# Kernel optimization log

Hardware: AMD Instinct MI355X
Metric: run time of the kernel (lower is better)

The kernel has to match this reference:

```python
import jax, jax.numpy as jnp
import numpy as np

DT = 1.0          # integration timestep (ms)
SIGMA = 0.5       # gauss_std for surrogate (unused in pure fwd spike)
AMPLITUDE = 0.3   # dampening_factor
N = 50000         # neurons
R = 4             # receptor types
D = 5             # max_delay
E = 5000000       # recurrent synapses
B = 4             # batch


def setup_inputs() -> dict:
    key = jax.random.key(0)
    ks = jax.random.split(key, 20)
    f = jnp.float32
    inputs = jax.random.normal(ks[0], (B, N * R), f) * 0.1
    # z_buf holds binary spikes for the last D steps
    z_buf = jax.random.bernoulli(ks[1], 0.05, (B, N * D)).astype(f)
    v = jax.random.uniform(ks[2], (B, N), f, 0.0, 1.0)
    r = jnp.zeros((B, N), f)
    asc_1 = jax.random.normal(ks[3], (B, N), f)
    asc_2 = jax.random.normal(ks[4], (B, N), f)
    psc_rise = jax.random.normal(ks[5], (B, N * R), f) * 0.5
    psc = jax.random.normal(ks[6], (B, N * R), f)
    rec_w = jax.random.normal(ks[7], (E,), f) * 0.01
    rec_rows = jax.random.randint(ks[8], (E,), 0, N * R, jnp.int32)
    rec_cols = jax.random.randint(ks[9], (E,), 0, N * D, jnp.int32)
    syn_decay = jax.random.uniform(ks[10], (N, R), f, 0.5, 0.99)
    psc_initial = jax.random.uniform(ks[11], (N, R), f, 0.1, 1.0)
    t_ref = jax.random.uniform(ks[12], (N,), f, 1.0, 4.0)
    asc_amps = jax.random.normal(ks[13], (N, 2), f)
    k = jax.random.normal(ks[14], (N, 2), f)  # inv-sigmoid space, read via sigmoid
    v_th = jnp.ones((N,), f)
    e_l = jnp.zeros((N,), f)
    v_reset = jnp.zeros((N,), f)
    g = jax.random.uniform(ks[15], (N,), f, 0.1, 1.0)
    decay = jax.random.uniform(ks[16], (N,), f, 0.8, 0.99)
    current_factor = jax.random.uniform(ks[17], (N,), f, 0.1, 1.0)
    voltage_scale = jnp.ones((N,), f) * 20.0
    voltage_offset = jnp.ones((N,), f) * -70.0
    return dict(inputs=inputs, z_buf=z_buf, v=v, r=r, asc_1=asc_1, asc_2=asc_2,
                psc_rise=psc_rise, psc=psc, rec_w=rec_w, rec_rows=rec_rows,
                rec_cols=rec_cols, syn_decay=syn_decay, psc_initial=psc_initial,
                t_ref=t_ref, asc_amps=asc_amps, k=k, v_th=v_th, e_l=e_l,
                v_reset=v_reset, g=g, decay=decay, current_factor=current_factor,
                voltage_scale=voltage_scale, voltage_offset=voltage_offset)


def _step(inputs, z_buf, v, r, asc_1, asc_2, psc_rise, psc,
          rec_w, rec_rows, rec_cols, syn_decay, psc_initial, t_ref,
          asc_amps, k, v_th, e_l, v_reset, g, decay, current_factor,
          voltage_scale, voltage_offset):
    shaped_z_buf = z_buf.reshape(B, D, N)
    prev_z = shaped_z_buf[:, 0]                      # most recent spikes [B,N]
    psc_rise_r = psc_rise.reshape(B, N, R)
    psc_r = psc.reshape(B, N, R)

    # sparse recurrent matmul: W[N*R, N*D] @ z_buf^T -> [N*R, B]
    vals = rec_w[:, None] * z_buf.T[rec_cols]        # [E, B] gather
    i_rec = jax.ops.segment_sum(vals, rec_rows, num_segments=N * R).T  # [B, N*R]

    rec_inputs = (i_rec + inputs).reshape(B, N, R)
    new_psc_rise = syn_decay * psc_rise_r + rec_inputs * psc_initial
    new_psc = psc_r * syn_decay + DT * syn_decay * psc_rise_r

    new_r = jax.nn.relu(r + prev_z * t_ref - DT)

    kk = jax.nn.sigmoid(k)                           # param_k_read()
    new_asc_1 = jnp.exp(-DT * kk[:, 0]) * asc_1 + prev_z * asc_amps[:, 0]
    new_asc_2 = jnp.exp(-DT * kk[:, 1]) * asc_2 + prev_z * asc_amps[:, 1]

    reset_current = prev_z * (v_reset - v_th)
    input_current = psc_r.sum(-1)                    # old psc
    c1 = input_current + asc_1 + asc_2 + g * e_l
    new_v = decay * v + current_factor * c1 + reset_current

    v_sc = (new_v - v_th) / (v_th - e_l)
    new_z = (v_sc > 0.0).astype(v_sc.dtype)          # spike_gauss forward
    new_z = jnp.where(new_r > 0.0, jnp.zeros_like(new_z), new_z)

    new_z_buf = jnp.concatenate([new_z[:, None], shaped_z_buf[:, :-1]], axis=1)
    out_v = new_v * voltage_scale + voltage_offset
    return (new_z, out_v, new_r, new_asc_1, new_asc_2,
            new_psc_rise.reshape(B, N * R), new_psc.reshape(B, N * R),
            new_z_buf.reshape(B, N * D))


def reference(inputs, z_buf, v, r, asc_1, asc_2, psc_rise, psc,
              rec_w, rec_rows, rec_cols, syn_decay, psc_initial, t_ref,
              asc_amps, k, v_th, e_l, v_reset, g, decay, current_factor,
              voltage_scale, voltage_offset):
    outs = _step(inputs, z_buf, v, r, asc_1, asc_2, psc_rise, psc,
                 rec_w, rec_rows, rec_cols, syn_decay, psc_initial, t_ref,
                 asc_amps, k, v_th, e_l, v_reset, g, decay, current_factor,
                 voltage_scale, voltage_offset)
    # pack outputs + new state into one [B, N*(5+2R+D)] array
    return jnp.concatenate(outs, axis=-1)
```

## Files before the change

### kernel.cpp

```cpp
#include <hip/hip_runtime.h>

#define Nn 50000
#define Rr 4
#define Dd 5
#define Ee 5000000
#define Bb 4
#define NRr (Nn * Rr)
#define NDd (Nn * Dd)
#define ZW 7814

struct P {
    const float* inputs; const float* z_buf; const float* v; const float* r;
    const float* asc1; const float* asc2; const float* psc_rise; const float* psc;
    const float* rec_w; const int* rec_rows; const int* rec_cols;
    const float* syn_decay; const float* psc_initial; const float* t_ref;
    const float* asc_amps; const float* k; const float* v_th; const float* e_l;
    const float* v_reset; const float* g; const float* decay;
    const float* current_factor; const float* vscale; const float* voffset;
    float* out; float* i_rec; unsigned char* z_pack; unsigned* zbits;
};

__global__ __launch_bounds__(256) void pack_z_kernel(P p) {
    int i = blockIdx.x * 256 + threadIdx.x;
    if (i < Bb * NRr / 4)
        ((float4*)p.i_rec)[i] = make_float4(0.f, 0.f, 0.f, 0.f);
    unsigned m = 0;
    if (i < NDd) {
#pragma unroll
        for (int b = 0; b < Bb; ++b)
            if (p.z_buf[(size_t)b * NDd + i] != 0.0f) m |= (1u << b);
        p.z_pack[i] = (unsigned char)m;
    }
    unsigned long long bal = __ballot(m != 0);
    if ((i & 63) == 0 && i < NDd) {
        p.zbits[(i >> 5)]     = (unsigned)bal;
        p.zbits[(i >> 5) + 1] = (unsigned)(bal >> 32);
    }
}

__global__ __launch_bounds__(256) void edge_neuron_kernel(P p) {
    __shared__ unsigned zb[ZW];
    for (int t = threadIdx.x; t < ZW; t += 256) zb[t] = p.zbits[t];
    __syncthreads();
    const int tid = blockIdx.x * 256 + threadIdx.x;

    if (tid < Bb * Nn) {
        int b = tid / Nn;
        int n = tid - b * Nn;
        const size_t bn  = (size_t)b * Nn + n;
        const size_t bnr = (size_t)b * NRr + (size_t)n * 4;

        float prev_z = p.z_buf[(size_t)b * NDd + n];
        float4 pr = *(const float4*)(p.psc_rise + bnr);
        float4 pc = *(const float4*)(p.psc + bnr);
        float4 sd = *(const float4*)(p.syn_decay + (size_t)n * 4);

        float4 npc;
        npc.x = pc.x * sd.x + sd.x * pr.x;
        npc.y = pc.y * sd.y + sd.y * pr.y;
        npc.z = pc.z * sd.z + sd.z * pr.z;
        npc.w = pc.w * sd.w + sd.w * pr.w;
        float input_current = pc.x + pc.y + pc.z + pc.w;

        float new_r = fmaxf(p.r[bn] + prev_z * p.t_ref[n] - 1.0f, 0.0f);

        float2 kv = *(const float2*)(p.k + (size_t)n * 2);
        float2 aa = *(const float2*)(p.asc_amps + (size_t)n * 2);
        float kk0 = 1.0f / (1.0f + expf(-kv.x));
        float kk1 = 1.0f / (1.0f + expf(-kv.y));
        float a1 = p.asc1[bn];
        float a2 = p.asc2[bn];
        float na1 = expf(-kk0) * a1 + prev_z * aa.x;
        float na2 = expf(-kk1) * a2 + prev_z * aa.y;

        float vth = p.v_th[n];
        float el  = p.e_l[n];
        float reset_current = prev_z * (p.v_reset[n] - vth);
        float c1 = input_current + a1 + a2 + p.g[n] * el;
        float new_v = p.decay[n] * p.v[bn] + p.current_factor[n] * c1
                      + reset_current;
        float v_sc = (new_v - vth) / (vth - el);
        float new_z = (v_sc > 0.0f) ? 1.0f : 0.0f;
        if (new_r > 0.0f) new_z = 0.0f;
        float out_v = new_v * p.vscale[n] + p.voffset[n];

        float* ob = p.out + (size_t)b * 18 * Nn;
        ob[n]          = new_z;
        ob[Nn + n]     = out_v;
        ob[2 * Nn + n] = new_r;
        ob[3 * Nn + n] = na1;
        ob[4 * Nn + n] = na2;
        *(float4*)(ob + 9 * Nn + (size_t)n * 4) = npc;
        ob[13 * Nn + n] = new_z;
#pragma unroll
        for (int d = 0; d < Dd - 1; ++d)
            ob[14 * Nn + (size_t)d * Nn + n] =
                p.z_buf[(size_t)b * NDd + (size_t)d * Nn + n];
    }

    if (tid < Ee / 4) {
        int4 c = ((const int4*)p.rec_cols)[tid];
        unsigned h0 = (zb[(unsigned)c.x >> 5] >> (c.x & 31)) & 1u;
        unsigned h1 = (zb[(unsigned)c.y >> 5] >> (c.y & 31)) & 1u;
        unsigned h2 = (zb[(unsigned)c.z >> 5] >> (c.z & 31)) & 1u;
        unsigned h3 = (zb[(unsigned)c.w >> 5] >> (c.w & 31)) & 1u;
        if (h0 | h1 | h2 | h3) {
            int4 rw = ((const int4*)p.rec_rows)[tid];
            float4 w = ((const float4*)p.rec_w)[tid];
            float* i_rec = p.i_rec;
            auto do_edge = [&](unsigned hh, int col, int row, float wv) {
                if (hh) {
                    unsigned mm = p.z_pack[col];
                    if (mm & 1u) atomicAdd(&i_rec[0 * NRr + row], wv);
                    if (mm & 2u) atomicAdd(&i_rec[1 * NRr + row], wv);
                    if (mm & 4u) atomicAdd(&i_rec[2 * NRr + row], wv);
                    if (mm & 8u) atomicAdd(&i_rec[3 * NRr + row], wv);
                }
            };
            do_edge(h0, c.x, rw.x, w.x);
            do_edge(h1, c.y, rw.y, w.y);
            do_edge(h2, c.z, rw.z, w.z);
            do_edge(h3, c.w, rw.w, w.w);
        }
    }
}

__global__ __launch_bounds__(256) void psc_rise_kernel(P p) {
    int tid = blockIdx.x * 256 + threadIdx.x;
    if (tid >= Bb * Nn) return;
    int b = tid / Nn;
    int n = tid - b * Nn;
    const size_t bnr = (size_t)b * NRr + (size_t)n * 4;
    float4 ir  = *(const float4*)(p.i_rec + bnr);
    float4 in4 = *(const float4*)(p.inputs + bnr);
    float4 pr  = *(const float4*)(p.psc_rise + bnr);
    float4 sd  = *(const float4*)(p.syn_decay + (size_t)n * 4);
    float4 pi  = *(const float4*)(p.psc_initial + (size_t)n * 4);
    float4 npr;
    npr.x = sd.x * pr.x + (ir.x + in4.x) * pi.x;
    npr.y = sd.y * pr.y + (ir.y + in4.y) * pi.y;
    npr.z = sd.z * pr.z + (ir.z + in4.z) * pi.z;
    npr.w = sd.w * pr.w + (ir.w + in4.w) * pi.w;
    float* ob = p.out + (size_t)b * 18 * Nn;
    *(float4*)(ob + 5 * Nn + (size_t)n * 4) = npr;
}

extern "C" void kernel_launch(void* const* d_in, const int* in_sizes, int n_in,
                              void* d_out, int out_size, void* d_ws, size_t ws_size,
                              hipStream_t stream) {
    P p;
    p.inputs        = (const float*)d_in[0];
    p.z_buf         = (const float*)d_in[1];
    p.v             = (const float*)d_in[2];
    p.r             = (const float*)d_in[3];
    p.asc1          = (const float*)d_in[4];
    p.asc2          = (const float*)d_in[5];
    p.psc_rise      = (const float*)d_in[6];
    p.psc           = (const float*)d_in[7];
    p.rec_w         = (const float*)d_in[8];
    p.rec_rows      = (const int*)d_in[9];
    p.rec_cols      = (const int*)d_in[10];
    p.syn_decay     = (const float*)d_in[11];
    p.psc_initial   = (const float*)d_in[12];
    p.t_ref         = (const float*)d_in[13];
    p.asc_amps      = (const float*)d_in[14];
    p.k             = (const float*)d_in[15];
    p.v_th          = (const float*)d_in[16];
    p.e_l           = (const float*)d_in[17];
    p.v_reset       = (const float*)d_in[18];
    p.g             = (const float*)d_in[19];
    p.decay         = (const float*)d_in[20];
    p.current_factor= (const float*)d_in[21];
    p.vscale        = (const float*)d_in[22];
    p.voffset       = (const float*)d_in[23];
    p.out           = (float*)d_out;
    p.i_rec  = (float*)d_ws;
    p.z_pack = (unsigned char*)d_ws + 3200000;
    p.zbits  = (unsigned*)((char*)d_ws + 3450240);

    pack_z_kernel<<<(NDd + 255) / 256, 256, 0, stream>>>(p);
    edge_neuron_kernel<<<(Ee / 4 + 255) / 256, 256, 0, stream>>>(p);
    psc_rise_kernel<<<(Bb * Nn + 255) / 256, 256, 0, stream>>>(p);
}
```

Baseline: 202.8 us.

## Scatter scaled recurrent current directly into output psc_rise slice

Computes the psc_rise base term (decay*psc_rise + inputs*psc_initial) in the neuron pass and has the edge kernel atomically add weight*psc_initial straight into the output psc_rise region. This removes the i_rec workspace, the zeroing pass and the third kernel launch with its extra read of i_rec. In exchange each atomic now also gathers psc_initial[row], and the neuron work moves into the pack kernel, which must finish before the edge kernel's atomics land.

```diff
diff --git a/kernel.cpp b/kernel.cpp
--- a/kernel.cpp
+++ b/kernel.cpp
@@ -8,6 +8,7 @@
 #define NRr (Nn * Rr)
 #define NDd (Nn * Dd)
 #define ZW 7814
+#define OUT_STRIDE (18 * Nn)
 
 struct P {
     const float* inputs; const float* z_buf; const float* v; const float* r;
@@ -17,13 +18,12 @@
     const float* asc_amps; const float* k; const float* v_th; const float* e_l;
     const float* v_reset; const float* g; const float* decay;
     const float* current_factor; const float* vscale; const float* voffset;
-    float* out; float* i_rec; unsigned char* z_pack; unsigned* zbits;
+    float* out; unsigned char* z_pack; unsigned* zbits;
 };
 
-__global__ __launch_bounds__(256) void pack_z_kernel(P p) {
+__global__ __launch_bounds__(256) void pack_neuron_kernel(P p) {
     int i = blockIdx.x * 256 + threadIdx.x;
-    if (i < Bb * NRr / 4)
-        ((float4*)p.i_rec)[i] = make_float4(0.f, 0.f, 0.f, 0.f);
+
     unsigned m = 0;
     if (i < NDd) {
 #pragma unroll
@@ -36,24 +36,25 @@
         p.zbits[(i >> 5)]     = (unsigned)bal;
         p.zbits[(i >> 5) + 1] = (unsigned)(bal >> 32);
     }
-}
 
-__global__ __launch_bounds__(256) void edge_neuron_kernel(P p) {
-    __shared__ unsigned zb[ZW];
-    for (int t = threadIdx.x; t < ZW; t += 256) zb[t] = p.zbits[t];
-    __syncthreads();
-    const int tid = blockIdx.x * 256 + threadIdx.x;
-
-    if (tid < Bb * Nn) {
-        int b = tid / Nn;
-        int n = tid - b * Nn;
+    if (i < Bb * Nn) {
+        int b = i / Nn;
+        int n = i - b * Nn;
         const size_t bn  = (size_t)b * Nn + n;
         const size_t bnr = (size_t)b * NRr + (size_t)n * 4;
 
         float prev_z = p.z_buf[(size_t)b * NDd + n];
-        float4 pr = *(const float4*)(p.psc_rise + bnr);
-        float4 pc = *(const float4*)(p.psc + bnr);
-        float4 sd = *(const float4*)(p.syn_decay + (size_t)n * 4);
+        float4 pr  = *(const float4*)(p.psc_rise + bnr);
+        float4 pc  = *(const float4*)(p.psc + bnr);
+        float4 in4 = *(const float4*)(p.inputs + bnr);
+        float4 sd  = *(const float4*)(p.syn_decay + (size_t)n * 4);
+        float4 pi  = *(const float4*)(p.psc_initial + (size_t)n * 4);
+
+        float4 nprb;
+        nprb.x = sd.x * pr.x + in4.x * pi.x;
+        nprb.y = sd.y * pr.y + in4.y * pi.y;
+        nprb.z = sd.z * pr.z + in4.z * pi.z;
+        nprb.w = sd.w * pr.w + in4.w * pi.w;
 
         float4 npc;
         npc.x = pc.x * sd.x + sd.x * pr.x;
@@ -84,12 +85,13 @@
         if (new_r > 0.0f) new_z = 0.0f;
         float out_v = new_v * p.vscale[n] + p.voffset[n];
 
-        float* ob = p.out + (size_t)b * 18 * Nn;
+        float* ob = p.out + (size_t)b * OUT_STRIDE;
         ob[n]          = new_z;
         ob[Nn + n]     = out_v;
         ob[2 * Nn + n] = new_r;
         ob[3 * Nn + n] = na1;
         ob[4 * Nn + n] = na2;
+        *(float4*)(ob + 5 * Nn + (size_t)n * 4) = nprb;
         *(float4*)(ob + 9 * Nn + (size_t)n * 4) = npc;
         ob[13 * Nn + n] = new_z;
 #pragma unroll
@@ -97,52 +99,41 @@
             ob[14 * Nn + (size_t)d * Nn + n] =
                 p.z_buf[(size_t)b * NDd + (size_t)d * Nn + n];
     }
-
-    if (tid < Ee / 4) {
-        int4 c = ((const int4*)p.rec_cols)[tid];
-        unsigned h0 = (zb[(unsigned)c.x >> 5] >> (c.x & 31)) & 1u;
-        unsigned h1 = (zb[(unsigned)c.y >> 5] >> (c.y & 31)) & 1u;
-        unsigned h2 = (zb[(unsigned)c.z >> 5] >> (c.z & 31)) & 1u;
-        unsigned h3 = (zb[(unsigned)c.w >> 5] >> (c.w & 31)) & 1u;
-        if (h0 | h1 | h2 | h3) {
-            int4 rw = ((const int4*)p.rec_rows)[tid];
-            float4 w = ((const float4*)p.rec_w)[tid];
-            float* i_rec = p.i_rec;
-            auto do_edge = [&](unsigned hh, int col, int row, float wv) {
-                if (hh) {
-                    unsigned mm = p.z_pack[col];
-                    if (mm & 1u) atomicAdd(&i_rec[0 * NRr + row], wv);
-                    if (mm & 2u) atomicAdd(&i_rec[1 * NRr + row], wv);
-                    if (mm & 4u) atomicAdd(&i_rec[2 * NRr + row], wv);
-                    if (mm & 8u) atomicAdd(&i_rec[3 * NRr + row], wv);
-                }
-            };
-            do_edge(h0, c.x, rw.x, w.x);
-            do_edge(h1, c.y, rw.y, w.y);
-            do_edge(h2, c.z, rw.z, w.z);
-            do_edge(h3, c.w, rw.w, w.w);
-        }
-    }
 }
 
-__global__ __launch_bounds__(256) void psc_rise_kernel(P p) {
-    int tid = blockIdx.x * 256 + threadIdx.x;
-    if (tid >= Bb * Nn) return;
-    int b = tid / Nn;
-    int n = tid - b * Nn;
-    const size_t bnr = (size_t)b * NRr + (size_t)n * 4;
-    float4 ir  = *(const float4*)(p.i_rec + bnr);
-    float4 in4 = *(const float4*)(p.inputs + bnr);
-    float4 pr  = *(const float4*)(p.psc_rise + bnr);
-    float4 sd  = *(const float4*)(p.syn_decay + (size_t)n * 4);
-    float4 pi  = *(const float4*)(p.psc_initial + (size_t)n * 4);
-    float4 npr;
-    npr.x = sd.x * pr.x + (ir.x + in4.x) * pi.x;
-    npr.y = sd.y * pr.y + (ir.y + in4.y) * pi.y;
-    npr.z = sd.z * pr.z + (ir.z + in4.z) * pi.z;
-    npr.w = sd.w * pr.w + (ir.w + in4.w) * pi.w;
-    float* ob = p.out + (size_t)b * 18 * Nn;
-    *(float4*)(ob + 5 * Nn + (size_t)n * 4) = npr;
+__global__ __launch_bounds__(256) void edge_kernel(P p) {
+    __shared__ unsigned zb[ZW];
+    for (int t = threadIdx.x; t < ZW; t += 256) zb[t] = p.zbits[t];
+    __syncthreads();
+    const int tid = blockIdx.x * 256 + threadIdx.x;
+    if (tid >= Ee / 4) return;
+
+    int4 c = ((const int4*)p.rec_cols)[tid];
+    unsigned h0 = (zb[(unsigned)c.x >> 5] >> (c.x & 31)) & 1u;
+    unsigned h1 = (zb[(unsigned)c.y >> 5] >> (c.y & 31)) & 1u;
+    unsigned h2 = (zb[(unsigned)c.z >> 5] >> (c.z & 31)) & 1u;
+    unsigned h3 = (zb[(unsigned)c.w >> 5] >> (c.w & 31)) & 1u;
+    if (!(h0 | h1 | h2 | h3)) return;
+
+    int4 rw = ((const int4*)p.rec_rows)[tid];
+    float4 w = ((const float4*)p.rec_w)[tid];
+    float* o5 = p.out + 5 * Nn;
+    auto do_edge = [&](unsigned hh, int col, int row, float wv) {
+        if (hh) {
+            unsigned mm = p.z_pack[col];
+            if (mm) {
+                float wp = wv * p.psc_initial[row];
+                if (mm & 1u) atomicAdd(o5 + 0 * OUT_STRIDE + row, wp);
+                if (mm & 2u) atomicAdd(o5 + 1 * OUT_STRIDE + row, wp);
+                if (mm & 4u) atomicAdd(o5 + 2 * OUT_STRIDE + row, wp);
+                if (mm & 8u) atomicAdd(o5 + 3 * OUT_STRIDE + row, wp);
+            }
+        }
+    };
+    do_edge(h0, c.x, rw.x, w.x);
+    do_edge(h1, c.y, rw.y, w.y);
+    do_edge(h2, c.z, rw.z, w.z);
+    do_edge(h3, c.w, rw.w, w.w);
 }
 
 extern "C" void kernel_launch(void* const* d_in, const int* in_sizes, int n_in,
@@ -174,11 +165,9 @@
     p.vscale        = (const float*)d_in[22];
     p.voffset       = (const float*)d_in[23];
     p.out           = (float*)d_out;
-    p.i_rec  = (float*)d_ws;
-    p.z_pack = (unsigned char*)d_ws + 3200000;
-    p.zbits  = (unsigned*)((char*)d_ws + 3450240);
+    p.z_pack = (unsigned char*)d_ws;
+    p.zbits  = (unsigned*)((char*)d_ws + ((NDd + 255) & ~255));
 
-    pack_z_kernel<<<(NDd + 255) / 256, 256, 0, stream>>>(p);
-    edge_neuron_kernel<<<(Ee / 4 + 255) / 256, 256, 0, stream>>>(p);
-    psc_rise_kernel<<<(Bb * Nn + 255) / 256, 256, 0, stream>>>(p);
+    pack_neuron_kernel<<<(NDd + 255) / 256, 256, 0, stream>>>(p);
+    edge_kernel<<<(Ee / 4 + 255) / 256, 256, 0, stream>>>(p);
 }
```

Result: no change. 204.7 us (+1.0%).

## Drop LDS spike bitmap, gather packed spike bytes directly, move neuron update to pack kernel

Applied to the files above, without the earlier changes.

Removes the ballot-built spike bitmap and the per-block LDS preload of about 31KB in the edge kernel. The edge kernel now gathers the per-column packed batch byte from global memory, which is about 250KB and likely cache-resident, and uses nontemporal loads for the streamed edge arrays. The neuron update moves into the pack kernel, leaving the edge kernel as a lean gather-and-atomic pass. The trade is that every edge now does four scattered byte loads from L2 instead of cheap LDS bit tests. In exchange, the block-level LDS fill and sync disappear, which should raise occupancy.

```diff
diff --git a/kernel.cpp b/kernel.cpp
--- a/kernel.cpp
+++ b/kernel.cpp
@@ -7,7 +7,10 @@
 #define Bb 4
 #define NRr (Nn * Rr)
 #define NDd (Nn * Dd)
-#define ZW 7814
+#define OUT_STRIDE (18 * Nn)
+
+typedef int   v4i __attribute__((ext_vector_type(4)));
+typedef float v4f __attribute__((ext_vector_type(4)));
 
 struct P {
     const float* inputs; const float* z_buf; const float* v; const float* r;
@@ -17,36 +20,26 @@
     const float* asc_amps; const float* k; const float* v_th; const float* e_l;
     const float* v_reset; const float* g; const float* decay;
     const float* current_factor; const float* vscale; const float* voffset;
-    float* out; float* i_rec; unsigned char* z_pack; unsigned* zbits;
+    float* out; float* i_rec; unsigned char* z_pack;
 };
 
-__global__ __launch_bounds__(256) void pack_z_kernel(P p) {
+__global__ __launch_bounds__(256) void pack_neuron_kernel(P p) {
     int i = blockIdx.x * 256 + threadIdx.x;
+
     if (i < Bb * NRr / 4)
         ((float4*)p.i_rec)[i] = make_float4(0.f, 0.f, 0.f, 0.f);
-    unsigned m = 0;
+
     if (i < NDd) {
+        unsigned m = 0;
 #pragma unroll
         for (int b = 0; b < Bb; ++b)
             if (p.z_buf[(size_t)b * NDd + i] != 0.0f) m |= (1u << b);
         p.z_pack[i] = (unsigned char)m;
     }
-    unsigned long long bal = __ballot(m != 0);
-    if ((i & 63) == 0 && i < NDd) {
-        p.zbits[(i >> 5)]     = (unsigned)bal;
-        p.zbits[(i >> 5) + 1] = (unsigned)(bal >> 32);
-    }
-}
 
-__global__ __launch_bounds__(256) void edge_neuron_kernel(P p) {
-    __shared__ unsigned zb[ZW];
-    for (int t = threadIdx.x; t < ZW; t += 256) zb[t] = p.zbits[t];
-    __syncthreads();
-    const int tid = blockIdx.x * 256 + threadIdx.x;
-
-    if (tid < Bb * Nn) {
-        int b = tid / Nn;
-        int n = tid - b * Nn;
+    if (i < Bb * Nn) {
+        int b = i / Nn;
+        int n = i - b * Nn;
         const size_t bn  = (size_t)b * Nn + n;
         const size_t bnr = (size_t)b * NRr + (size_t)n * 4;
 
@@ -84,7 +77,7 @@
         if (new_r > 0.0f) new_z = 0.0f;
         float out_v = new_v * p.vscale[n] + p.voffset[n];
 
-        float* ob = p.out + (size_t)b * 18 * Nn;
+        float* ob = p.out + (size_t)b * OUT_STRIDE;
         ob[n]          = new_z;
         ob[Nn + n]     = out_v;
         ob[2 * Nn + n] = new_r;
@@ -97,32 +90,32 @@
             ob[14 * Nn + (size_t)d * Nn + n] =
                 p.z_buf[(size_t)b * NDd + (size_t)d * Nn + n];
     }
+}
 
-    if (tid < Ee / 4) {
-        int4 c = ((const int4*)p.rec_cols)[tid];
-        unsigned h0 = (zb[(unsigned)c.x >> 5] >> (c.x & 31)) & 1u;
-        unsigned h1 = (zb[(unsigned)c.y >> 5] >> (c.y & 31)) & 1u;
-        unsigned h2 = (zb[(unsigned)c.z >> 5] >> (c.z & 31)) & 1u;
-        unsigned h3 = (zb[(unsigned)c.w >> 5] >> (c.w & 31)) & 1u;
-        if (h0 | h1 | h2 | h3) {
-            int4 rw = ((const int4*)p.rec_rows)[tid];
-            float4 w = ((const float4*)p.rec_w)[tid];
-            float* i_rec = p.i_rec;
-            auto do_edge = [&](unsigned hh, int col, int row, float wv) {
-                if (hh) {
-                    unsigned mm = p.z_pack[col];
-                    if (mm & 1u) atomicAdd(&i_rec[0 * NRr + row], wv);
-                    if (mm & 2u) atomicAdd(&i_rec[1 * NRr + row], wv);
-                    if (mm & 4u) atomicAdd(&i_rec[2 * NRr + row], wv);
-                    if (mm & 8u) atomicAdd(&i_rec[3 * NRr + row], wv);
-                }
-            };
-            do_edge(h0, c.x, rw.x, w.x);
-            do_edge(h1, c.y, rw.y, w.y);
-            do_edge(h2, c.z, rw.z, w.z);
-            do_edge(h3, c.w, rw.w, w.w);
-        }
-    }
+__global__ __launch_bounds__(256) void edge_kernel(P p) {
+    int tid = blockIdx.x * 256 + threadIdx.x;
+    if (tid >= Ee / 4) return;
+
+    v4i c = __builtin_nontemporal_load(&((const v4i*)p.rec_cols)[tid]);
+    unsigned m0 = p.z_pack[c.x];
+    unsigned m1 = p.z_pack[c.y];
+    unsigned m2 = p.z_pack[c.z];
+    unsigned m3 = p.z_pack[c.w];
+    if (!(m0 | m1 | m2 | m3)) return;
+
+    v4i rw = __builtin_nontemporal_load(&((const v4i*)p.rec_rows)[tid]);
+    v4f w  = __builtin_nontemporal_load(&((const v4f*)p.rec_w)[tid]);
+    float* i_rec = p.i_rec;
+    auto do_edge = [&](unsigned mm, int row, float wv) {
+        if (mm & 1u) atomicAdd(&i_rec[0 * NRr + row], wv);
+        if (mm & 2u) atomicAdd(&i_rec[1 * NRr + row], wv);
+        if (mm & 4u) atomicAdd(&i_rec[2 * NRr + row], wv);
+        if (mm & 8u) atomicAdd(&i_rec[3 * NRr + row], wv);
+    };
+    do_edge(m0, rw.x, w.x);
+    do_edge(m1, rw.y, w.y);
+    do_edge(m2, rw.z, w.z);
+    do_edge(m3, rw.w, w.w);
 }
 
 __global__ __launch_bounds__(256) void psc_rise_kernel(P p) {
@@ -141,7 +134,7 @@
     npr.y = sd.y * pr.y + (ir.y + in4.y) * pi.y;
     npr.z = sd.z * pr.z + (ir.z + in4.z) * pi.z;
     npr.w = sd.w * pr.w + (ir.w + in4.w) * pi.w;
-    float* ob = p.out + (size_t)b * 18 * Nn;
+    float* ob = p.out + (size_t)b * OUT_STRIDE;
     *(float4*)(ob + 5 * Nn + (size_t)n * 4) = npr;
 }
 
@@ -174,11 +167,11 @@
     p.vscale        = (const float*)d_in[22];
     p.voffset       = (const float*)d_in[23];
     p.out           = (float*)d_out;
+
     p.i_rec  = (float*)d_ws;
     p.z_pack = (unsigned char*)d_ws + 3200000;
-    p.zbits  = (unsigned*)((char*)d_ws + 3450240);
 
-    pack_z_kernel<<<(NDd + 255) / 256, 256, 0, stream>>>(p);
-    edge_neuron_kernel<<<(Ee / 4 + 255) / 256, 256, 0, stream>>>(p);
+    pack_neuron_kernel<<<(NDd + 255) / 256, 256, 0, stream>>>(p);
+    edge_kernel<<<(Ee / 4 + 255) / 256, 256, 0, stream>>>(p);
     psc_rise_kernel<<<(Bb * Nn + 255) / 256, 256, 0, stream>>>(p);
 }
```

Result: slower. 208.6 us (+2.9%).
